# Optimization experiments

Hardware: AMD Instinct MI355X
Metric: run time of the kernel (lower is better)

Reference implementation:

```python
import jax, jax.numpy as jnp
import numpy as np

N = 50000   # nodes
E = 400000  # edges per metapath
M = 3       # metapaths
L = 2       # HAN layers
IN = 256    # input feat = hidden*heads so layers stack
H = 4       # heads
DO = 64     # out per head
D = H * DO  # 256


def setup_inputs() -> dict:
    key = jax.random.key(0)
    ks = jax.random.split(key, 12)
    x = jax.random.normal(ks[0], (M, N, IN), jnp.float32)
    src = jax.random.randint(ks[1], (M, E), 0, N, jnp.int32)
    dst = jax.random.randint(ks[2], (M, E), 0, N, jnp.int32)
    W_gat = jax.random.normal(ks[3], (L, M, IN, D), jnp.float32) * 0.06
    attn_l = jax.random.normal(ks[4], (L, M, H, DO), jnp.float32) * 0.1
    attn_r = jax.random.normal(ks[5], (L, M, H, DO), jnp.float32) * 0.1
    bias_gat = jnp.zeros((L, M, D), jnp.float32)
    W1 = jax.random.normal(ks[6], (D, DO), jnp.float32) * 0.06
    b1 = jnp.zeros((DO,), jnp.float32)
    W2 = jax.random.normal(ks[7], (DO, 1), jnp.float32) * 0.1
    Wp = jax.random.normal(ks[8], (D, DO), jnp.float32) * 0.06
    bp = jnp.zeros((DO,), jnp.float32)
    return {"x": x, "W_gat": W_gat, "attn_l": attn_l, "attn_r": attn_r,
            "bias_gat": bias_gat, "W1": W1, "b1": b1, "W2": W2,
            "Wp": Wp, "bp": bp, "src": src, "dst": dst}


def gat_conv(h, src, dst, W, al, ar, bias):
    # h: (N, IN) -> feat: (N, H, DO)
    feat = (h @ W).reshape(N, H, DO)
    el = jnp.einsum('nhd,hd->nh', feat, al)   # (N, H)
    er = jnp.einsum('nhd,hd->nh', feat, ar)   # (N, H)
    e = jax.nn.leaky_relu(el[src] + er[dst], 0.2)  # (E, H)
    # numerically stable edge softmax over incoming edges per dst node
    mx = jax.ops.segment_max(e, dst, num_segments=N)  # (N, H)
    mx = jnp.where(jnp.isfinite(mx), mx, 0.0)         # empty segments
    ex = jnp.exp(e - mx[dst])                         # (E, H)
    denom = jax.ops.segment_sum(ex, dst, num_segments=N)  # (N, H)
    msg = jax.ops.segment_sum(ex[:, :, None] * feat[src], dst, num_segments=N)  # (N,H,DO)
    out = msg / jnp.maximum(denom, 1e-9)[:, :, None]
    out = out + bias.reshape(H, DO)
    return jax.nn.elu(out).reshape(N, D)  # flatten(1)


def reference(x, W_gat, attn_l, attn_r, bias_gat, W1, b1, W2, Wp, bp, src, dst):
    h = [x[i] for i in range(M)]
    for l in range(L):
        h = [gat_conv(h[i], src[i], dst[i], W_gat[l, i], attn_l[l, i],
                      attn_r[l, i], bias_gat[l, i]) for i in range(M)]
    z = jnp.stack(h, axis=1)  # (N, M, D)
    # semantic attention: small MLP -> per-metapath scalar, softmax over M
    w = (jnp.tanh(z @ W1 + b1) @ W2).mean(0)   # (M, 1)
    beta = jax.nn.softmax(w, axis=0)           # (M, 1)
    agg = (z * beta[None]).sum(1)              # (N, D)
    return agg @ Wp + bp                       # (N, DO)
```

## Files before the change

### kernel.cpp

```cpp
#include <hip/hip_runtime.h>

#define NN 50000
#define EE 400000
#define MM 3
#define CHUNK 2048
#define NCHUNK ((NN + CHUNK - 1) / CHUNK)

typedef float f32x4 __attribute__((ext_vector_type(4)));
typedef short s16x8 __attribute__((ext_vector_type(8)));
typedef _Float16 half_t;
typedef _Float16 h16x4 __attribute__((ext_vector_type(4)));

union FU { float f; unsigned u; };

__device__ inline short bfhi(float x) {
    FU c; c.f = x;
    unsigned u = c.u;
    return (short)((u + 0x7fffu + ((u >> 16) & 1u)) >> 16);
}
__device__ inline float bf2f(short h) {
    FU c; c.u = ((unsigned)(unsigned short)h) << 16;
    return c.f;
}
__device__ inline float h2f(short bits) {
    union HU { short s; _Float16 h; } u; u.s = bits; return (float)u.h;
}

__device__ inline void glds16(const void* g, void* l) {
    __builtin_amdgcn_global_load_lds(
        (const __attribute__((address_space(1))) void*)g,
        (__attribute__((address_space(3))) void*)l, 16, 0, 0);
}


__global__ __launch_bounds__(256) void init_kernel(int* counts, float* wsum) {
    int idx = blockIdx.x * 256 + threadIdx.x;
    if (idx < MM * NN) counts[idx] = 0;
    if (idx < MM) wsum[idx] = 0.0f;
}

__global__ __launch_bounds__(256) void hist_kernel(const int* __restrict__ dst,
                                                   int* __restrict__ counts) {
    int m = blockIdx.y;
    int e = blockIdx.x * 256 + threadIdx.x;
    if (e < EE) atomicAdd(&counts[m * NN + dst[m * EE + e]], 1);
}

__global__ __launch_bounds__(256) void scan_partial_kernel(const int* __restrict__ counts,
                                                           int* __restrict__ rp,
                                                           int* __restrict__ bsum) {
    int m = blockIdx.y, ch = blockIdx.x;
    const int* c = counts + m * NN;
    int* r = rp + m * (NN + 1);
    int t = threadIdx.x, lane = t & 63, wave = t >> 6;
    int i0 = ch * CHUNK + t * 8;
    int v[8]; int s = 0;
#pragma unroll
    for (int k = 0; k < 8; ++k) { int i = i0 + k; v[k] = (i < NN) ? c[i] : 0; s += v[k]; }
    int incl = s;
#pragma unroll
    for (int off = 1; off < 64; off <<= 1) {
        int u = __shfl_up(incl, off);
        if (lane >= off) incl += u;
    }
    int excl = incl - s;
    __shared__ int wsh[4];
    if (lane == 63) wsh[wave] = incl;
    __syncthreads();
    int woff = 0;
    for (int w = 0; w < wave; ++w) woff += wsh[w];
    int run = excl + woff;
#pragma unroll
    for (int k = 0; k < 8; ++k) { int i = i0 + k; if (i < NN) r[i] = run; run += v[k]; }
    if (t == 255) bsum[m * NCHUNK + ch] = woff + incl;
}

__global__ __launch_bounds__(256) void scan_top_kernel(int* __restrict__ bsum) {
    int wave = threadIdx.x >> 6, lane = threadIdx.x & 63;
    if (wave < MM) {
        int v = (lane < NCHUNK) ? bsum[wave * NCHUNK + lane] : 0;
        int incl = v;
#pragma unroll
        for (int off = 1; off < 64; off <<= 1) {
            int u = __shfl_up(incl, off);
            if (lane >= off) incl += u;
        }
        if (lane < NCHUNK) bsum[wave * NCHUNK + lane] = incl - v;
    }
}

__global__ __launch_bounds__(256) void scan_add_kernel(const int* __restrict__ bsum,
                                                       int* __restrict__ rp,
                                                       int* __restrict__ cur) {
    int m = blockIdx.y, ch = blockIdx.x;
    int off = bsum[m * NCHUNK + ch];
    int* r = rp + m * (NN + 1);
    int* q = cur + m * (NN + 1);
    int i0 = ch * CHUNK + threadIdx.x * 8;
#pragma unroll
    for (int k = 0; k < 8; ++k) {
        int i = i0 + k;
        if (i < NN) { int val = r[i] + off; r[i] = val; q[i] = val; }
    }
    if (ch == 0 && threadIdx.x == 0) r[NN] = EE;
}

__global__ __launch_bounds__(256) void scatter_kernel(const int* __restrict__ src,
                                                      const int* __restrict__ dst,
                                                      int* __restrict__ cursor,
                                                      long long* __restrict__ spair) {
    int m = blockIdx.y;
    int e = blockIdx.x * 256 + threadIdx.x;
    if (e < EE) {
        int d = dst[m * EE + e];
        int pos = atomicAdd(&cursor[m * (NN + 1) + d], 1);
        long long p = ((long long)d << 32) | (unsigned)src[m * EE + e];
        __builtin_nontemporal_store(p, &spair[(size_t)m * EE + pos]);
    }
}


#define WG_ELEMS (6 * 256 * 256)
#define W_TOT (WG_ELEMS + 128 * 256)

__global__ __launch_bounds__(256) void splitW_kernel(const float* __restrict__ Wg,
                                                     const float* __restrict__ W1,
                                                     const float* __restrict__ Wp,
                                                     short* __restrict__ Whi,
                                                     short* __restrict__ Wlo) {
    int idx = blockIdx.x * 256 + threadIdx.x;
    if (idx >= W_TOT) return;
    float v;
    if (idx < WG_ELEMS) {
        int mat = idx >> 16;
        int rem = idx & 65535;
        int kb  = rem >> 13;
        int r2  = rem & 8191;
        int n   = r2 >> 5;
        int s5  = r2 & 31;
        int cc  = s5 >> 3;
        int jj  = s5 & 7;
        int c   = cc ^ ((n >> 1) & 3);
        int k   = kb * 32 + c * 8 + jj;
        v = Wg[mat * 65536 + k * 256 + n];
    } else {
        int i2 = idx - WG_ELEMS;
        int n = i2 >> 8, k = i2 & 255;
        v = (n < 64) ? W1[k * 64 + n] : Wp[k * 64 + n - 64];
    }
    short h = bfhi(v);
    Whi[idx] = h;
    Wlo[idx] = bfhi(v - bf2f(h));
}


template<int AMODE>
__global__ __launch_bounds__(256) void mfma_gemm(
    const float* __restrict__ Af, const half_t* __restrict__ A16,
    const short* __restrict__ Wthi, const short* __restrict__ Wtlo,
    half_t* __restrict__ featA,
    const float* __restrict__ alA, const float* __restrict__ arA,
    float* __restrict__ elA, float* __restrict__ erA) {
    __shared__ short Ah[64 * 32], Al[64 * 32], Bh[256 * 32], Bl[256 * 32];
    const int m = blockIdx.y;
    const int t = threadIdx.x;
    const int lane = t & 63;
    const int wn = t >> 6;
    const int row0 = blockIdx.x * 64;
    const float*  A0 = Af + (size_t)m * NN * 256;
    const short*  A1 = (const short*)(A16 + (size_t)m * NN * 256);
    const char*   BghB = (const char*)(Wthi + (size_t)m * 65536);
    const char*   BglB = (const char*)(Wtlo + (size_t)m * 65536);
    half_t* Ch = featA + (size_t)m * NN * 256;
    const float* al = alA + m * 256;
    const float* ar = arA + m * 256;
    float* el = elA + (size_t)m * NN * 4;
    float* er = erA + (size_t)m * NN * 4;
    f32x4 acc[4][4] = {};

    const int r = t >> 2, c0 = t & 3;
    const int aoff = r * 32 + ((c0 ^ ((r >> 1) & 3)) << 3);
    const int arow = row0 + r;
    const bool aval = (arow < NN);
    const int cb = wn * 4096;

    s16x8 pr0 = {0,0,0,0,0,0,0,0}, pr1 = {0,0,0,0,0,0,0,0};
    float4 a00 = make_float4(0.f,0.f,0.f,0.f), a01 = a00, a10 = a00, a11 = a00;

    if (AMODE == 1) {
        if (aval) {
            pr0 = *(const s16x8*)(A1 + (size_t)arow * 256 + c0 * 8);
            pr1 = *(const s16x8*)(A1 + (size_t)arow * 256 + 32 + c0 * 8);
        }
    } else {
        if (aval) {
            a00 = *(const float4*)(A0 + (size_t)arow * 256 + c0 * 8);
            a01 = *(const float4*)(A0 + (size_t)arow * 256 + c0 * 8 + 4);
            a10 = *(const float4*)(A0 + (size_t)arow * 256 + 32 + c0 * 8);
            a11 = *(const float4*)(A0 + (size_t)arow * 256 + 32 + c0 * 8 + 4);
        }
    }

    for (int kb = 0; kb < 8; ++kb) {
        {
            float v[8];
            if (AMODE == 1) {
#pragma unroll
                for (int j = 0; j < 8; ++j) v[j] = h2f(pr0[j]);
            } else {
                v[0] = a00.x; v[1] = a00.y; v[2] = a00.z; v[3] = a00.w;
                v[4] = a01.x; v[5] = a01.y; v[6] = a01.z; v[7] = a01.w;
            }
            s16x8 hh, ll;
#pragma unroll
            for (int j = 0; j < 8; ++j) {
                short hs = bfhi(v[j]);
                hh[j] = hs;
                ll[j] = bfhi(v[j] - bf2f(hs));
            }
            *(s16x8*)&Ah[aoff] = hh;
            *(s16x8*)&Al[aoff] = ll;
        }
        if (AMODE == 1) {
            pr0 = pr1;
            pr1 = s16x8{0,0,0,0,0,0,0,0};
            if (kb + 2 < 8 && aval)
                pr1 = *(const s16x8*)(A1 + (size_t)arow * 256 + (kb + 2) * 32 + c0 * 8);
        } else {
            a00 = a10; a01 = a11;
            a10 = make_float4(0.f,0.f,0.f,0.f); a11 = a10;
            if (kb + 2 < 8 && aval) {
                a10 = *(const float4*)(A0 + (size_t)arow * 256 + (kb + 2) * 32 + c0 * 8);
                a11 = *(const float4*)(A0 + (size_t)arow * 256 + (kb + 2) * 32 + c0 * 8 + 4);
            }
        }
        {
            const char* sh = BghB + kb * 16384 + cb;
            const char* sl = BglB + kb * 16384 + cb;
            char* dh = (char*)&Bh[0] + cb;
            char* dl = (char*)&Bl[0] + cb;
#pragma unroll
            for (int u = 0; u < 4; ++u) {
                glds16(sh + u * 1024 + lane * 16, dh + u * 1024);
                glds16(sl + u * 1024 + lane * 16, dl + u * 1024);
            }
        }
        __syncthreads();
        int fr = lane & 15, ac = lane >> 4;
        s16x8 afh[4], afl[4], bfh[4], bfl[4];
#pragma unroll
        for (int i = 0; i < 4; ++i) {
            int rr = i * 16 + fr;
            int off = rr * 32 + ((ac ^ ((rr >> 1) & 3)) << 3);
            afh[i] = *(const s16x8*)&Ah[off];
            afl[i] = *(const s16x8*)&Al[off];
        }
#pragma unroll
        for (int j = 0; j < 4; ++j) {
            int n = wn * 64 + j * 16 + fr;
            int off = n * 32 + ((ac ^ ((n >> 1) & 3)) << 3);
            bfh[j] = *(const s16x8*)&Bh[off];
            bfl[j] = *(const s16x8*)&Bl[off];
        }
#pragma unroll
        for (int i = 0; i < 4; ++i)
#pragma unroll
            for (int j = 0; j < 4; ++j) {
                acc[i][j] = __builtin_amdgcn_mfma_f32_16x16x32_bf16(afh[i], bfh[j], acc[i][j], 0, 0, 0);
                acc[i][j] = __builtin_amdgcn_mfma_f32_16x16x32_bf16(afh[i], bfl[j], acc[i][j], 0, 0, 0);
                acc[i][j] = __builtin_amdgcn_mfma_f32_16x16x32_bf16(afl[i], bfh[j], acc[i][j], 0, 0, 0);
            }
        __syncthreads();
    }

#pragma unroll
    for (int i = 0; i < 4; ++i) {
        int rbase = row0 + i * 16 + (lane >> 4) * 4;
#pragma unroll
        for (int j = 0; j < 4; ++j) {
            int col = wn * 64 + j * 16 + (lane & 15);
#pragma unroll
            for (int q = 0; q < 4; ++q) {
                int row = rbase + q;
                if (row < NN) Ch[(size_t)row * 256 + col] = (half_t)acc[i][j][q];
            }
        }
    }
    float alv[4], arv[4];
#pragma unroll
    for (int j = 0; j < 4; ++j) {
        int col = wn * 64 + j * 16 + (lane & 15);
        alv[j] = al[col];
        arv[j] = ar[col];
    }
#pragma unroll
    for (int i = 0; i < 4; ++i)
#pragma unroll
        for (int q = 0; q < 4; ++q) {
            float ep = acc[i][0][q] * alv[0] + acc[i][1][q] * alv[1]
                     + acc[i][2][q] * alv[2] + acc[i][3][q] * alv[3];
            float rp_ = acc[i][0][q] * arv[0] + acc[i][1][q] * arv[1]
                      + acc[i][2][q] * arv[2] + acc[i][3][q] * arv[3];
#pragma unroll
            for (int msk = 1; msk < 16; msk <<= 1) {
                ep += __shfl_xor(ep, msk);
                rp_ += __shfl_xor(rp_, msk);
            }
            if ((lane & 15) == 0) {
                int row = row0 + i * 16 + (lane >> 4) * 4 + q;
                if (row < NN) {
                    el[row * 4 + wn] = ep;
                    er[row * 4 + wn] = rp_;
                }
            }
        }
}


__global__ __launch_bounds__(256) void sem_gemm(
    const half_t* __restrict__ A16,
    const short* __restrict__ Wthi, const short* __restrict__ Wtlo,
    float* __restrict__ P,
    const float* __restrict__ b1, const float* __restrict__ w2,
    float* __restrict__ wsum,
    int nrows) {
    __shared__ short Ah[128 * 32], Al[128 * 32], Bh[128 * 32], Bl[128 * 32];
    const int t = threadIdx.x;
    const int lane = t & 63;
    const int wave = t >> 6;
    const int wm = wave >> 1, wn = wave & 1;
    const int row0 = blockIdx.x * 128;
    const short* A1 = (const short*)A16;
    f32x4 acc[4][4] = {};

    const int r0 = (t * 2) >> 2, c0 = (t * 2) & 3;
    const int r1 = (t * 2 + 1) >> 2, c1 = (t * 2 + 1) & 3;
    const int aoff0 = r0 * 32 + ((c0 ^ ((r0 >> 1) & 3)) << 3);
    const int aoff1 = r1 * 32 + ((c1 ^ ((r1 >> 1) & 3)) << 3);
    const int arow0 = row0 + r0, arow1 = row0 + r1;

    s16x8 p0 = {0,0,0,0,0,0,0,0}, p1 = {0,0,0,0,0,0,0,0};
    if (arow0 < nrows) p0 = *(const s16x8*)(A1 + (size_t)arow0 * 256 + c0 * 8);
    if (arow1 < nrows) p1 = *(const s16x8*)(A1 + (size_t)arow1 * 256 + c1 * 8);

    for (int k0 = 0; k0 < 256; k0 += 32) {
        {
            s16x8 hh, ll;
#pragma unroll
            for (int j = 0; j < 8; ++j) {
                float v = h2f(p0[j]);
                short hs = bfhi(v);
                hh[j] = hs; ll[j] = bfhi(v - bf2f(hs));
            }
            *(s16x8*)&Ah[aoff0] = hh; *(s16x8*)&Al[aoff0] = ll;
#pragma unroll
            for (int j = 0; j < 8; ++j) {
                float v = h2f(p1[j]);
                short hs = bfhi(v);
                hh[j] = hs; ll[j] = bfhi(v - bf2f(hs));
            }
            *(s16x8*)&Ah[aoff1] = hh; *(s16x8*)&Al[aoff1] = ll;
        }
#pragma unroll
        for (int u = 0; u < 2; ++u) {
            int idx = t * 2 + u;
            int n = idx >> 2, c = idx & 3;
            s16x8 h = *(const s16x8*)(Wthi + (size_t)n * 256 + k0 + c * 8);
            s16x8 l = *(const s16x8*)(Wtlo + (size_t)n * 256 + k0 + c * 8);
            int off = n * 32 + ((c ^ ((n >> 1) & 3)) << 3);
            *(s16x8*)&Bh[off] = h;
            *(s16x8*)&Bl[off] = l;
        }
        __syncthreads();
        if (k0 + 32 < 256) {
            p0 = s16x8{0,0,0,0,0,0,0,0}; p1 = s16x8{0,0,0,0,0,0,0,0};
            if (arow0 < nrows) p0 = *(const s16x8*)(A1 + (size_t)arow0 * 256 + k0 + 32 + c0 * 8);
            if (arow1 < nrows) p1 = *(const s16x8*)(A1 + (size_t)arow1 * 256 + k0 + 32 + c1 * 8);
        }
        int fr = lane & 15, ac = lane >> 4;
        s16x8 afh[4], afl[4], bfh[4], bfl[4];
#pragma unroll
        for (int i = 0; i < 4; ++i) {
            int rr = wm * 64 + i * 16 + fr;
            int off = rr * 32 + ((ac ^ ((rr >> 1) & 3)) << 3);
            afh[i] = *(const s16x8*)&Ah[off];
            afl[i] = *(const s16x8*)&Al[off];
        }
#pragma unroll
        for (int j = 0; j < 4; ++j) {
            int n = wn * 64 + j * 16 + fr;
            int off = n * 32 + ((ac ^ ((n >> 1) & 3)) << 3);
            bfh[j] = *(const s16x8*)&Bh[off];
            bfl[j] = *(const s16x8*)&Bl[off];
        }
#pragma unroll
        for (int i = 0; i < 4; ++i)
#pragma unroll
            for (int j = 0; j < 4; ++j) {
                acc[i][j] = __builtin_amdgcn_mfma_f32_16x16x32_bf16(afh[i], bfh[j], acc[i][j], 0, 0, 0);
                acc[i][j] = __builtin_amdgcn_mfma_f32_16x16x32_bf16(afh[i], bfl[j], acc[i][j], 0, 0, 0);
                acc[i][j] = __builtin_amdgcn_mfma_f32_16x16x32_bf16(afl[i], bfh[j], acc[i][j], 0, 0, 0);
            }
        __syncthreads();
    }

    float* wp = (float*)&Ah[0];
    if (t < 3) wp[t] = 0.f;
    __syncthreads();
    int fr = lane & 15, ac = lane >> 4;
    if (wn == 0) {
        float b1v[4], w2v[4];
#pragma unroll
        for (int j = 0; j < 4; ++j) {
            int col = j * 16 + fr;
            b1v[j] = b1[col];
            w2v[j] = w2[col];
        }
#pragma unroll
        for (int i = 0; i < 4; ++i)
#pragma unroll
            for (int q = 0; q < 4; ++q) {
                float ep = tanhf(acc[i][0][q] + b1v[0]) * w2v[0]
                         + tanhf(acc[i][1][q] + b1v[1]) * w2v[1]
                         + tanhf(acc[i][2][q] + b1v[2]) * w2v[2]
                         + tanhf(acc[i][3][q] + b1v[3]) * w2v[3];
#pragma unroll
                for (int msk = 1; msk < 16; msk <<= 1) ep += __shfl_xor(ep, msk);
                if (fr == 0) {
                    int row = row0 + wm * 64 + i * 16 + ac * 4 + q;
                    if (row < nrows) atomicAdd(&wp[row / NN], ep);
                }
            }
    } else {
#pragma unroll
        for (int i = 0; i < 4; ++i) {
            int rbase = row0 + wm * 64 + i * 16 + ac * 4;
#pragma unroll
            for (int j = 0; j < 4; ++j) {
                int pcol = j * 16 + fr;
#pragma unroll
                for (int q = 0; q < 4; ++q) {
                    int row = rbase + q;
                    if (row < nrows) P[(size_t)row * 64 + pcol] = acc[i][j][q];
                }
            }
        }
    }
    __syncthreads();
    if (t < 3) atomicAdd(&wsum[t], wp[t]);
}


__global__ __launch_bounds__(256) void agg_edges_kernel(const half_t* __restrict__ featA,
                                                        const float* __restrict__ elA,
                                                        const float* __restrict__ erA,
                                                        const int* __restrict__ row_ptrA,
                                                        const long long* __restrict__ spairA,
                                                        const float* __restrict__ biasL,
                                                        half_t* __restrict__ HbA) {
    const int m = blockIdx.y;
    const half_t* feat = featA + (size_t)m * NN * 256;
    const float* el = elA + (size_t)m * NN * 4;
    const float* er = erA + (size_t)m * NN * 4;
    const int* row_ptr = row_ptrA + (size_t)m * (NN + 1);
    const long long* spair = spairA + (size_t)m * EE;
    const float* bias = biasL + m * 256;
    half_t* out = HbA + (size_t)m * NN * 256;

    int wave = threadIdx.x >> 6;
    int lane = threadIdx.x & 63;
    int n = blockIdx.x * 4 + wave;
    int h = lane >> 4;
    int beg = row_ptr[n], end = row_ptr[n + 1];
    float ern = er[n * 4 + h];
    const h16x4* fb = (const h16x4*)feat + lane;
    float a0A = 0.f, a1A = 0.f, a2A = 0.f, a3A = 0.f, dA = 0.f;
    float a0B = 0.f, a1B = 0.f, a2B = 0.f, a3B = 0.f, dB = 0.f;
    float a0C = 0.f, a1C = 0.f, a2C = 0.f, a3C = 0.f, dC = 0.f;
    float a0D = 0.f, a1D = 0.f, a2D = 0.f, a3D = 0.f, dD = 0.f;
    int j = beg;
    for (; j + 3 < end; j += 4) {
        int sA = (int)(unsigned)spair[j];
        int sB = (int)(unsigned)spair[j + 1];
        int sC = (int)(unsigned)spair[j + 2];
        int sD = (int)(unsigned)spair[j + 3];
        float eA = el[sA * 4 + h] + ern; eA = eA > 0.f ? eA : 0.2f * eA; float wA = __expf(eA);
        float eB = el[sB * 4 + h] + ern; eB = eB > 0.f ? eB : 0.2f * eB; float wB = __expf(eB);
        float eC = el[sC * 4 + h] + ern; eC = eC > 0.f ? eC : 0.2f * eC; float wC = __expf(eC);
        float eD = el[sD * 4 + h] + ern; eD = eD > 0.f ? eD : 0.2f * eD; float wD = __expf(eD);
        h16x4 fA = fb[(size_t)sA * 64];
        h16x4 fB = fb[(size_t)sB * 64];
        h16x4 fC = fb[(size_t)sC * 64];
        h16x4 fD = fb[(size_t)sD * 64];
        a0A = fmaf(wA, (float)fA.x, a0A); a1A = fmaf(wA, (float)fA.y, a1A);
        a2A = fmaf(wA, (float)fA.z, a2A); a3A = fmaf(wA, (float)fA.w, a3A); dA += wA;
        a0B = fmaf(wB, (float)fB.x, a0B); a1B = fmaf(wB, (float)fB.y, a1B);
        a2B = fmaf(wB, (float)fB.z, a2B); a3B = fmaf(wB, (float)fB.w, a3B); dB += wB;
        a0C = fmaf(wC, (float)fC.x, a0C); a1C = fmaf(wC, (float)fC.y, a1C);
        a2C = fmaf(wC, (float)fC.z, a2C); a3C = fmaf(wC, (float)fC.w, a3C); dC += wC;
        a0D = fmaf(wD, (float)fD.x, a0D); a1D = fmaf(wD, (float)fD.y, a1D);
        a2D = fmaf(wD, (float)fD.z, a2D); a3D = fmaf(wD, (float)fD.w, a3D); dD += wD;
    }
    for (; j < end; ++j) {
        int s = (int)(unsigned)spair[j];
        float e = el[s * 4 + h] + ern;
        e = e > 0.f ? e : 0.2f * e;
        float w = __expf(e);
        h16x4 f = fb[(size_t)s * 64];
        a0A = fmaf(w, (float)f.x, a0A); a1A = fmaf(w, (float)f.y, a1A);
        a2A = fmaf(w, (float)f.z, a2A); a3A = fmaf(w, (float)f.w, a3A); dA += w;
    }
    float den = fmaxf((dA + dB) + (dC + dD), 1e-9f);
    int col = lane * 4;
    float o0 = ((a0A + a0B) + (a0C + a0D)) / den + bias[col + 0];
    float o1 = ((a1A + a1B) + (a1C + a1D)) / den + bias[col + 1];
    float o2 = ((a2A + a2B) + (a2C + a2D)) / den + bias[col + 2];
    float o3 = ((a3A + a3B) + (a3C + a3D)) / den + bias[col + 3];
    o0 = o0 > 0.f ? o0 : __expf(o0) - 1.0f;
    o1 = o1 > 0.f ? o1 : __expf(o1) - 1.0f;
    o2 = o2 > 0.f ? o2 : __expf(o2) - 1.0f;
    o3 = o3 > 0.f ? o3 : __expf(o3) - 1.0f;
    h16x4 ov; ov.x = (half_t)o0; ov.y = (half_t)o1; ov.z = (half_t)o2; ov.w = (half_t)o3;
    ((h16x4*)(out + (size_t)n * 256))[lane] = ov;
}


__global__ void beta_kernel(const float* __restrict__ wsum, float* __restrict__ beta) {
    if (threadIdx.x == 0 && blockIdx.x == 0) {
        float w0 = wsum[0] / (float)NN, w1 = wsum[1] / (float)NN, w2 = wsum[2] / (float)NN;
        float mx = fmaxf(w0, fmaxf(w1, w2));
        float e0 = __expf(w0 - mx), e1 = __expf(w1 - mx), e2 = __expf(w2 - mx);
        float s = e0 + e1 + e2;
        beta[0] = e0 / s; beta[1] = e1 / s; beta[2] = e2 / s;
    }
}

__global__ __launch_bounds__(256) void combine_out_kernel(const float* __restrict__ P,
                                                          const float* __restrict__ beta,
                                                          const float* __restrict__ bp,
                                                          float* __restrict__ out) {
    int idx4 = blockIdx.x * 256 + threadIdx.x;
    if (idx4 >= NN * 64 / 4) return;
    float b0 = beta[0], b1 = beta[1], b2 = beta[2];
    float4 p0 = ((const float4*)P)[idx4];
    float4 p1 = ((const float4*)P)[idx4 + NN * 16];
    float4 p2 = ((const float4*)P)[idx4 + NN * 32];
    float4 bpv = *(const float4*)(bp + ((idx4 * 4) & 63));
    float4 o;
    o.x = b0 * p0.x + b1 * p1.x + b2 * p2.x + bpv.x;
    o.y = b0 * p0.y + b1 * p1.y + b2 * p2.y + bpv.y;
    o.z = b0 * p0.z + b1 * p1.z + b2 * p2.z + bpv.z;
    o.w = b0 * p0.w + b1 * p1.w + b2 * p2.w + bpv.w;
    ((float4*)out)[idx4] = o;
}


extern "C" void kernel_launch(void* const* d_in, const int* in_sizes, int n_in,
                              void* d_out, int out_size, void* d_ws, size_t ws_size,
                              hipStream_t stream) {
    const float* x        = (const float*)d_in[0];
    const float* W_gat    = (const float*)d_in[1];
    const float* attn_l   = (const float*)d_in[2];
    const float* attn_r   = (const float*)d_in[3];
    const float* bias_gat = (const float*)d_in[4];
    const float* W1       = (const float*)d_in[5];
    const float* b1       = (const float*)d_in[6];
    const float* W2       = (const float*)d_in[7];
    const float* Wp       = (const float*)d_in[8];
    const float* bp       = (const float*)d_in[9];
    const int*   src      = (const int*)d_in[10];
    const int*   dst      = (const int*)d_in[11];
    float* out = (float*)d_out;

    char* ws = (char*)d_ws;
    size_t off = 0;
    auto alloc = [&](size_t bytes) { size_t o = off; off = (off + bytes + 255) & ~(size_t)255; return o; };
    half_t* Hb      = (half_t*)(ws + alloc((size_t)MM * NN * 256 * 2));
    half_t* feat    = (half_t*)(ws + alloc((size_t)MM * NN * 256 * 2));
    float*  P       = (float*)(ws + alloc((size_t)MM * NN * 64 * 4));
    float*  el      = (float*)(ws + alloc((size_t)MM * NN * 4 * 4));
    float*  er      = (float*)(ws + alloc((size_t)MM * NN * 4 * 4));
    int*    counts  = (int*)(ws + alloc((size_t)MM * NN * 4));
    int*    row_ptr = (int*)(ws + alloc((size_t)MM * (NN + 1) * 4));
    int*    cursor  = (int*)(ws + alloc((size_t)MM * (NN + 1) * 4));
    long long* spair = (long long*)(ws + alloc((size_t)MM * EE * 8));
    int*    bsum    = (int*)(ws + alloc((size_t)MM * NCHUNK * 4));
    short*  Whi     = (short*)(ws + alloc((size_t)W_TOT * 2));
    short*  Wlo     = (short*)(ws + alloc((size_t)W_TOT * 2));
    float*  wsum    = (float*)(ws + alloc(16));
    float*  beta    = (float*)(ws + alloc(16));

    init_kernel<<<dim3((MM * NN + 255) / 256), 256, 0, stream>>>(counts, wsum);
    hist_kernel<<<dim3((EE + 255) / 256, MM), 256, 0, stream>>>(dst, counts);
    scan_partial_kernel<<<dim3(NCHUNK, MM), 256, 0, stream>>>(counts, row_ptr, bsum);
    scan_top_kernel<<<dim3(1), 256, 0, stream>>>(bsum);
    scan_add_kernel<<<dim3(NCHUNK, MM), 256, 0, stream>>>(bsum, row_ptr, cursor);
    scatter_kernel<<<dim3((EE + 255) / 256, MM), 256, 0, stream>>>(src, dst, cursor, spair);
    splitW_kernel<<<dim3((W_TOT + 255) / 256), 256, 0, stream>>>(W_gat, W1, Wp, Whi, Wlo);

    const int rowTiles = (NN + 63) / 64;

    for (int l = 0; l < 2; ++l) {
        const short* wh = Whi + (size_t)l * MM * 65536;
        const short* wl = Wlo + (size_t)l * MM * 65536;
        const float* alp = attn_l + (size_t)l * MM * 256;
        const float* arp = attn_r + (size_t)l * MM * 256;
        if (l == 0)
            mfma_gemm<0><<<dim3(rowTiles, MM), 256, 0, stream>>>(
                x, nullptr, wh, wl, feat, alp, arp, el, er);
        else
            mfma_gemm<1><<<dim3(rowTiles, MM), 256, 0, stream>>>(
                nullptr, Hb, wh, wl, feat, alp, arp, el, er);
        agg_edges_kernel<<<dim3(NN / 4, MM), 256, 0, stream>>>(
            feat, el, er, row_ptr, spair, bias_gat + (size_t)l * MM * 256, Hb);
    }

    sem_gemm<<<dim3((MM * NN + 127) / 128), 256, 0, stream>>>(
        Hb, Whi + WG_ELEMS, Wlo + WG_ELEMS, P, b1, W2, wsum, MM * NN);
    beta_kernel<<<dim3(1), 64, 0, stream>>>(wsum, beta);
    combine_out_kernel<<<dim3((NN * 16 + 255) / 256), 256, 0, stream>>>(P, beta, bp, out);
}
```

Measured before the change: 657.7 us.

## Double GEMM row tile to 128 with 8 waves and register-staged B loads

The feature-projection GEMM now processes 128 rows per block with 512 threads (a 2x4 wave grid), so each staged B tile in LDS is reused across twice as many rows. The direct global-to-LDS loads of pre-swizzled weights are replaced with ordinary vector loads through registers that apply the XOR swizzle on the LDS write. The weight split kernel now stores plain transposed weights. This halves B traffic per output row, at the cost of larger LDS use, fewer blocks, and loss of the async LDS load path.

```diff
diff --git a/kernel.cpp b/kernel.cpp
--- a/kernel.cpp
+++ b/kernel.cpp
@@ -24,12 +24,6 @@
 }
 __device__ inline float h2f(short bits) {
     union HU { short s; _Float16 h; } u; u.s = bits; return (float)u.h;
-}
-
-__device__ inline void glds16(const void* g, void* l) {
-    __builtin_amdgcn_global_load_lds(
-        (const __attribute__((address_space(1))) void*)g,
-        (__attribute__((address_space(3))) void*)l, 16, 0, 0);
 }
 
 
@@ -132,16 +126,8 @@
     if (idx >= W_TOT) return;
     float v;
     if (idx < WG_ELEMS) {
-        int mat = idx >> 16;
-        int rem = idx & 65535;
-        int kb  = rem >> 13;
-        int r2  = rem & 8191;
-        int n   = r2 >> 5;
-        int s5  = r2 & 31;
-        int cc  = s5 >> 3;
-        int jj  = s5 & 7;
-        int c   = cc ^ ((n >> 1) & 3);
-        int k   = kb * 32 + c * 8 + jj;
+        int mat = idx >> 16, rem = idx & 65535;
+        int n = rem >> 8, k = rem & 255;
         v = Wg[mat * 65536 + k * 256 + n];
     } else {
         int i2 = idx - WG_ELEMS;
@@ -155,22 +141,23 @@
 
 
 template<int AMODE>
-__global__ __launch_bounds__(256) void mfma_gemm(
+__global__ __launch_bounds__(512) void mfma_gemm(
     const float* __restrict__ Af, const half_t* __restrict__ A16,
     const short* __restrict__ Wthi, const short* __restrict__ Wtlo,
     half_t* __restrict__ featA,
     const float* __restrict__ alA, const float* __restrict__ arA,
     float* __restrict__ elA, float* __restrict__ erA) {
-    __shared__ short Ah[64 * 32], Al[64 * 32], Bh[256 * 32], Bl[256 * 32];
+    __shared__ short Ah[128 * 32], Al[128 * 32], Bh[256 * 32], Bl[256 * 32];
     const int m = blockIdx.y;
     const int t = threadIdx.x;
     const int lane = t & 63;
-    const int wn = t >> 6;
-    const int row0 = blockIdx.x * 64;
+    const int wave = t >> 6;
+    const int wm = wave >> 2, wn = wave & 3;
+    const int row0 = blockIdx.x * 128;
     const float*  A0 = Af + (size_t)m * NN * 256;
     const short*  A1 = (const short*)(A16 + (size_t)m * NN * 256);
-    const char*   BghB = (const char*)(Wthi + (size_t)m * 65536);
-    const char*   BglB = (const char*)(Wtlo + (size_t)m * 65536);
+    const short*  Bgh = Wthi + (size_t)m * 65536;
+    const short*  Bgl = Wtlo + (size_t)m * 65536;
     half_t* Ch = featA + (size_t)m * NN * 256;
     const float* al = alA + m * 256;
     const float* ar = arA + m * 256;
@@ -182,7 +169,6 @@
     const int aoff = r * 32 + ((c0 ^ ((r >> 1) & 3)) << 3);
     const int arow = row0 + r;
     const bool aval = (arow < NN);
-    const int cb = wn * 4096;
 
     s16x8 pr0 = {0,0,0,0,0,0,0,0}, pr1 = {0,0,0,0,0,0,0,0};
     float4 a00 = make_float4(0.f,0.f,0.f,0.f), a01 = a00, a10 = a00, a11 = a00;
@@ -202,6 +188,7 @@
     }
 
     for (int kb = 0; kb < 8; ++kb) {
+        const int k0 = kb * 32;
         {
             float v[8];
             if (AMODE == 1) {
@@ -234,23 +221,22 @@
                 a11 = *(const float4*)(A0 + (size_t)arow * 256 + (kb + 2) * 32 + c0 * 8 + 4);
             }
         }
-        {
-            const char* sh = BghB + kb * 16384 + cb;
-            const char* sl = BglB + kb * 16384 + cb;
-            char* dh = (char*)&Bh[0] + cb;
-            char* dl = (char*)&Bl[0] + cb;
-#pragma unroll
-            for (int u = 0; u < 4; ++u) {
-                glds16(sh + u * 1024 + lane * 16, dh + u * 1024);
-                glds16(sl + u * 1024 + lane * 16, dl + u * 1024);
-            }
+#pragma unroll
+        for (int u = 0; u < 2; ++u) {
+            int idx = t * 2 + u;
+            int n = idx >> 2, c = idx & 3;
+            s16x8 h = *(const s16x8*)(Bgh + (size_t)n * 256 + k0 + c * 8);
+            s16x8 l = *(const s16x8*)(Bgl + (size_t)n * 256 + k0 + c * 8);
+            int off = n * 32 + ((c ^ ((n >> 1) & 3)) << 3);
+            *(s16x8*)&Bh[off] = h;
+            *(s16x8*)&Bl[off] = l;
         }
         __syncthreads();
         int fr = lane & 15, ac = lane >> 4;
         s16x8 afh[4], afl[4], bfh[4], bfl[4];
 #pragma unroll
         for (int i = 0; i < 4; ++i) {
-            int rr = i * 16 + fr;
+            int rr = wm * 64 + i * 16 + fr;
             int off = rr * 32 + ((ac ^ ((rr >> 1) & 3)) << 3);
             afh[i] = *(const s16x8*)&Ah[off];
             afl[i] = *(const s16x8*)&Al[off];
@@ -275,7 +261,7 @@
 
 #pragma unroll
     for (int i = 0; i < 4; ++i) {
-        int rbase = row0 + i * 16 + (lane >> 4) * 4;
+        int rbase = row0 + wm * 64 + i * 16 + (lane >> 4) * 4;
 #pragma unroll
         for (int j = 0; j < 4; ++j) {
             int col = wn * 64 + j * 16 + (lane & 15);
@@ -307,7 +293,7 @@
                 rp_ += __shfl_xor(rp_, msk);
             }
             if ((lane & 15) == 0) {
-                int row = row0 + i * 16 + (lane >> 4) * 4 + q;
+                int row = row0 + wm * 64 + i * 16 + (lane >> 4) * 4 + q;
                 if (row < NN) {
                     el[row * 4 + wn] = ep;
                     er[row * 4 + wn] = rp_;
@@ -598,7 +584,7 @@
     scatter_kernel<<<dim3((EE + 255) / 256, MM), 256, 0, stream>>>(src, dst, cursor, spair);
     splitW_kernel<<<dim3((W_TOT + 255) / 256), 256, 0, stream>>>(W_gat, W1, Wp, Whi, Wlo);
 
-    const int rowTiles = (NN + 63) / 64;
+    const int rowTiles = (NN + 127) / 128;
 
     for (int l = 0; l < 2; ++l) {
         const short* wh = Whi + (size_t)l * MM * 65536;
@@ -606,10 +592,10 @@
         const float* alp = attn_l + (size_t)l * MM * 256;
         const float* arp = attn_r + (size_t)l * MM * 256;
         if (l == 0)
-            mfma_gemm<0><<<dim3(rowTiles, MM), 256, 0, stream>>>(
+            mfma_gemm<0><<<dim3(rowTiles, MM), 512, 0, stream>>>(
                 x, nullptr, wh, wl, feat, alp, arp, el, er);
         else
-            mfma_gemm<1><<<dim3(rowTiles, MM), 256, 0, stream>>>(
+            mfma_gemm<1><<<dim3(rowTiles, MM), 512, 0, stream>>>(
                 nullptr, Hb, wh, wl, feat, alp, arp, el, er);
         agg_edges_kernel<<<dim3(NN / 4, MM), 256, 0, stream>>>(
             feat, el, er, row_ptr, spair, bias_gat + (size_t)l * MM * 256, Hb);
```

Result: slower. 689.4 us (+4.8%).
